# Kernel tuning notes

Measured on AMD Instinct MI355X. Metric: run time of the kernel, lower is better.

Reference implementation:

```python
import jax, jax.numpy as jnp
import numpy as np

# ---- static configuration (matches init_kwargs) ----
B = 32
H = 56
W = 56
C = 192
HEADS = 6
WS = 7            # window size
SHIFT = 3         # shift size (WS // 2)
MLP_HIDDEN = 768  # 4 * C
CPB = 256         # clip(56*56//16, 256, 1024)
N = WS * WS       # tokens per window
NW = (H // WS) * (W // WS)  # windows per image
EPS = 1e-5

# ---- static tables (Swin V2 continuous relative position bias) ----
# log-spaced relative coords table: [(2*WS-1)^2, 2]
_r = np.arange(-(WS - 1), WS, dtype=np.float32)
_tab = np.stack(np.meshgrid(_r, _r, indexing='ij'), axis=-1)  # [2WS-1, 2WS-1, 2]
_tab = _tab / (WS - 1) * 8.0  # pretrained_window_size=0 -> use window_size-1
_tab = np.sign(_tab) * np.log2(np.abs(_tab) + 1.0) / np.log2(8.0)
REL_TABLE = jnp.asarray(_tab.reshape(-1, 2))

# relative position index: [N, N] into the (2WS-1)^2 table
_coords = np.stack(np.meshgrid(np.arange(WS), np.arange(WS), indexing='ij'))
_cf = _coords.reshape(2, -1)
_rel = (_cf[:, :, None] - _cf[:, None, :]).transpose(1, 2, 0).astype(np.int64)
_rel[..., 0] += WS - 1
_rel[..., 1] += WS - 1
_rel[..., 0] *= 2 * WS - 1
REL_INDEX = jnp.asarray(_rel.sum(-1))

# shifted-window attention mask: [NW, N, N] with 0 / -100
_img = np.zeros((H, W), dtype=np.float32)
_sl = [slice(0, -WS), slice(-WS, -SHIFT), slice(-SHIFT, None)]
_cnt = 0
for _hs in _sl:
    for _ws in _sl:
        _img[_hs, _ws] = _cnt
        _cnt += 1
_mw = _img.reshape(H // WS, WS, W // WS, WS).transpose(0, 2, 1, 3).reshape(-1, N)
_am = _mw[:, None, :] - _mw[:, :, None]
ATTN_MASK = jnp.asarray(np.where(_am != 0, -100.0, 0.0).astype(np.float32))


def _layer_norm(x, g, b):
    mu = jnp.mean(x, axis=-1, keepdims=True)
    var = jnp.mean(jnp.square(x - mu), axis=-1, keepdims=True)
    return (x - mu) * jax.lax.rsqrt(var + EPS) * g + b


def setup_inputs() -> dict:
    key = jax.random.key(0)
    ks = jax.random.split(key, 10)
    def n(k, shape, s=0.02):
        return jax.random.normal(k, shape, jnp.float32) * s
    return {
        'x': jax.random.normal(ks[0], (B, H * W, C), jnp.float32),
        'qkv_w': n(ks[1], (3 * C, C)),
        'q_bias': jnp.zeros((C,), jnp.float32),
        'v_bias': jnp.zeros((C,), jnp.float32),
        'logit_scale': jnp.full((HEADS, 1, 1), jnp.log(10.0), jnp.float32),
        'cpb_w1': n(ks[2], (CPB, 2)),
        'cpb_b1': jnp.zeros((CPB,), jnp.float32),
        'cpb_w2': n(ks[3], (HEADS, CPB)),
        'proj_w': n(ks[4], (C, C)),
        'proj_b': jnp.zeros((C,), jnp.float32),
        'norm1_g': jnp.ones((C,), jnp.float32),
        'norm1_b': jnp.zeros((C,), jnp.float32),
        'norm2_g': jnp.ones((C,), jnp.float32),
        'norm2_b': jnp.zeros((C,), jnp.float32),
        'fc1_w': n(ks[5], (MLP_HIDDEN, C)),
        'fc1_b': jnp.zeros((MLP_HIDDEN,), jnp.float32),
        'fc2_w': n(ks[6], (C, MLP_HIDDEN)),
        'fc2_b': jnp.zeros((C,), jnp.float32),
    }


def reference(x, qkv_w, q_bias, v_bias, logit_scale, cpb_w1, cpb_b1, cpb_w2,
              proj_w, proj_b, norm1_g, norm1_b, norm2_g, norm2_b,
              fc1_w, fc1_b, fc2_w, fc2_b):
    b = x.shape[0]
    hd = C // HEADS
    shortcut = x

    # cyclic shift + window partition -> [b*NW, N, C]
    xi = jnp.roll(x.reshape(b, H, W, C), (-SHIFT, -SHIFT), axis=(1, 2))
    xw = xi.reshape(b, H // WS, WS, W // WS, WS, C)
    xw = xw.transpose(0, 1, 3, 2, 4, 5).reshape(-1, N, C)

    # qkv projection (k has no bias, per Swin V2)
    qkv_bias = jnp.concatenate([q_bias, jnp.zeros_like(q_bias), v_bias])
    qkv = (xw @ qkv_w.T + qkv_bias).reshape(-1, N, 3, HEADS, hd)
    qkv = qkv.transpose(2, 0, 3, 1, 4)  # [3, bw, heads, N, hd]
    q, k, v = qkv[0], qkv[1], qkv[2]

    # cosine attention with learned logit scale
    q = q / jnp.maximum(jnp.linalg.norm(q, axis=-1, keepdims=True), 1e-12)
    k = k / jnp.maximum(jnp.linalg.norm(k, axis=-1, keepdims=True), 1e-12)
    scale = jnp.exp(jnp.minimum(logit_scale, jnp.log(100.0)))  # [heads,1,1]
    attn = jnp.einsum('bhnd,bhmd->bhnm', q, k) * scale

    # continuous relative position bias via tiny MLP
    tab = jax.nn.relu(REL_TABLE @ cpb_w1.T + cpb_b1) @ cpb_w2.T  # [(2WS-1)^2, heads]
    rpb = 16.0 * jax.nn.sigmoid(tab[REL_INDEX])                  # [N, N, heads]
    attn = attn + rpb.transpose(2, 0, 1)[None]

    # shifted-window mask + softmax
    attn = attn.reshape(-1, NW, HEADS, N, N) + ATTN_MASK[None, :, None]
    attn = jax.nn.softmax(attn.reshape(-1, HEADS, N, N), axis=-1)

    out = jnp.einsum('bhnm,bhmd->bhnd', attn, v)
    out = out.transpose(0, 2, 1, 3).reshape(-1, N, C) @ proj_w.T + proj_b

    # window reverse + reverse shift
    xr = out.reshape(b, H // WS, W // WS, WS, WS, C)
    xr = xr.transpose(0, 1, 3, 2, 4, 5).reshape(b, H, W, C)
    xr = jnp.roll(xr, (SHIFT, SHIFT), axis=(1, 2)).reshape(b, H * W, C)

    # post-norm residual (Swin V2 style)
    x1 = shortcut + _layer_norm(xr, norm1_g, norm1_b)
    hmid = jax.nn.silu(x1 @ fc1_w.T + fc1_b) @ fc2_w.T + fc2_b
    return x1 + _layer_norm(hmid, norm2_g, norm2_b)
```

## Files before the change

### kernel.cpp

```cpp
#include <hip/hip_runtime.h>


typedef unsigned short ushort_t;
using f32x4  = __attribute__((ext_vector_type(4))) float;
using short8 = __attribute__((ext_vector_type(8))) short;

__device__ __forceinline__ ushort_t f2bf(float f) {
  union { float f; unsigned u; } v; v.f = f;
  unsigned r = v.u + 0x7fffu + ((v.u >> 16) & 1u);
  return (ushort_t)(r >> 16);
}
__device__ __forceinline__ float bf2f(ushort_t u) {
  union { unsigned u; float f; } v; v.u = ((unsigned)u) << 16;
  return v.f;
}

__device__ __forceinline__ int img_pos(int m) {
  int win = m / 49, n = m - win * 49;
  int b = win >> 6, wi = win & 63;
  int nd = n / 7, nm = n - nd * 7;
  int hs = (wi >> 3) * 7 + nd;
  int ws = (wi & 7) * 7 + nm;
  int h = hs + 3; if (h >= 56) h -= 56;
  int w = ws + 3; if (w >= 56) w -= 56;
  return b * 3136 + h * 56 + w;
}

__device__ __forceinline__ int region3(int a) { return a < 49 ? 0 : (a < 53 ? 1 : 2); }

__global__ void cvt_kernel(const float* __restrict__ in, ushort_t* __restrict__ out, int n) {
  int i = blockIdx.x * 256 + threadIdx.x;
  if (i < n) out[i] = f2bf(in[i]);
}

__global__ __launch_bounds__(256) void gather_cvt_kernel(
    const float* __restrict__ x, ushort_t* __restrict__ xw) {
  int i8 = blockIdx.x * 256 + threadIdx.x;
  int m = i8 / 24, c8 = (i8 - m * 24) * 8;
  const float* p = x + (size_t)img_pos(m) * 192 + c8;
  float4 a = *(const float4*)p, b = *(const float4*)(p + 4);
  ushort_t* q = xw + (size_t)m * 192 + c8;
  *(ushort4*)q       = make_ushort4(f2bf(a.x), f2bf(a.y), f2bf(a.z), f2bf(a.w));
  *(ushort4*)(q + 4) = make_ushort4(f2bf(b.x), f2bf(b.y), f2bf(b.z), f2bf(b.w));
}

__global__ __launch_bounds__(256) void cpb_kernel(
    const float* __restrict__ w1, const float* __restrict__ b1,
    const float* __restrict__ w2, float* __restrict__ tab_s) {
  int e = blockIdx.x;
  int t = threadIdx.x;
  int i = e / 13, j = e - 13 * (e / 13);
  auto cval = [](int a) -> float {
    float r = (a - 6) * (8.0f / 6.0f);
    float v = log2f(fabsf(r) + 1.f) * (1.f / 3.f);
    return r < 0.f ? -v : v;
  };
  float ci = cval(i), cj = cval(j);
  float h = fmaxf(ci * w1[2 * t] + cj * w1[2 * t + 1] + b1[t], 0.f);
  __shared__ float red[256];
  for (int head = 0; head < 6; ++head) {
    red[t] = h * w2[head * 256 + t];
    __syncthreads();
    for (int st = 128; st > 0; st >>= 1) {
      if (t < st) red[t] += red[t + st];
      __syncthreads();
    }
    if (t == 0) tab_s[head * 169 + e] = 16.f / (1.f + __expf(-red[0]));
    __syncthreads();
  }
}

template<int KTOT, int MODE>
__global__ __launch_bounds__(256) void gemm_n192(
    const ushort_t* __restrict__ Ab, const ushort_t* __restrict__ W,
    const float* __restrict__ b0, const float* __restrict__ b1,
    ushort_t* out, float* outf, int NTOT) {
  __shared__ ushort_t Al[128][40];
  __shared__ ushort_t Bl[192][40];
  int t = threadIdx.x;
  int m0 = blockIdx.x * 128, n0 = blockIdx.y * 192;

  int arow = t >> 1, akoff = (t & 1) << 4;
  const ushort_t* Arowp = Ab + (size_t)(m0 + arow) * KTOT + akoff;
  int colA = akoff ? 4 : 0;

  int lane = t & 63, wid = t >> 6;
  int wm = wid >> 1, wn = wid & 1;
  int lr = lane & 15, lg = lane >> 4;

  int bn = t >> 2, cB = t & 3;
  const ushort_t* Browp = W + (size_t)(n0 + bn) * KTOT + (cB << 3);
  const ushort_t* Browp2 = W + (size_t)(n0 + 64 + bn) * KTOT + (cB << 3);
  const ushort_t* Browp3 = W + (size_t)(n0 + 128 + bn) * KTOT + (cB << 3);
  int colB = ((cB & 1) << 4) | ((cB >> 1) << 2);

  f32x4 acc[4][6];
#pragma unroll
  for (int a = 0; a < 4; ++a)
#pragma unroll
    for (int b = 0; b < 6; ++b) acc[a][b] = (f32x4){0.f, 0.f, 0.f, 0.f};

  ushort4 a0, a1, a2, a3, bq0[2], bq1[2], bq2[2];
  auto LOADREGS = [&](int kt) {
    a0 = *(const ushort4*)(Arowp + kt + 0);
    a1 = *(const ushort4*)(Arowp + kt + 4);
    a2 = *(const ushort4*)(Arowp + kt + 8);
    a3 = *(const ushort4*)(Arowp + kt + 12);
    bq0[0] = *(const ushort4*)(Browp + kt);
    bq0[1] = *(const ushort4*)(Browp + kt + 4);
    bq1[0] = *(const ushort4*)(Browp2 + kt);
    bq1[1] = *(const ushort4*)(Browp2 + kt + 4);
    bq2[0] = *(const ushort4*)(Browp3 + kt);
    bq2[1] = *(const ushort4*)(Browp3 + kt + 4);
  };

  const int NT = KTOT / 32;
  LOADREGS(0);
  for (int it = 0; it < NT; ++it) {
    ushort_t* Ar = &Al[arow][0];
    *(ushort4*)(Ar + colA +  0) = a0;
    *(ushort4*)(Ar + colA +  8) = a1;
    *(ushort4*)(Ar + colA + 16) = a2;
    *(ushort4*)(Ar + colA + 24) = a3;
    ushort_t* Br0 = &Bl[bn][0];
    *(ushort4*)(Br0 + colB + 0) = bq0[0];
    *(ushort4*)(Br0 + colB + 8) = bq0[1];
    ushort_t* Br1 = &Bl[64 + bn][0];
    *(ushort4*)(Br1 + colB + 0) = bq1[0];
    *(ushort4*)(Br1 + colB + 8) = bq1[1];
    ushort_t* Br2 = &Bl[128 + bn][0];
    *(ushort4*)(Br2 + colB + 0) = bq2[0];
    *(ushort4*)(Br2 + colB + 8) = bq2[1];
    __syncthreads();
    if (it + 1 < NT) LOADREGS((it + 1) * 32);
    short8 af[4], bfv[6];
#pragma unroll
    for (int fm = 0; fm < 4; ++fm)
      af[fm] = *(const short8*)&Al[wm * 64 + fm * 16 + lr][lg * 8];
#pragma unroll
    for (int fn = 0; fn < 6; ++fn)
      bfv[fn] = *(const short8*)&Bl[wn * 96 + fn * 16 + lr][lg * 8];
#pragma unroll
    for (int fm = 0; fm < 4; ++fm)
#pragma unroll
      for (int fn = 0; fn < 6; ++fn)
        acc[fm][fn] = __builtin_amdgcn_mfma_f32_16x16x32_bf16(af[fm], bfv[fn], acc[fm][fn], 0, 0, 0);
    if (it + 1 < NT) __syncthreads();
  }
#pragma unroll
  for (int fm = 0; fm < 4; ++fm) {
#pragma unroll
    for (int fn = 0; fn < 6; ++fn) {
      int col = n0 + wn * 96 + fn * 16 + lr;
      float bias;
      if (MODE == 0) bias = (col < 192) ? b0[col] : ((col < 384) ? 0.f : b1[col - 384]);
      else           bias = b0[col];
#pragma unroll
      for (int r = 0; r < 4; ++r) {
        int row = m0 + wm * 64 + fm * 16 + lg * 4 + r;
        float v = acc[fm][fn][r] + bias;
        if (MODE == 1) v = v / (1.f + __expf(-v));
        if (MODE == 3) outf[(size_t)row * NTOT + col] = v;
        else           out[(size_t)row * NTOT + col] = f2bf(v);
      }
    }
  }
}

template<int MODE>
__global__ __launch_bounds__(256) void ln_resid_kernel(
    const ushort_t* __restrict__ pre, const float* __restrict__ residf,
    const ushort_t* __restrict__ residb, const float* __restrict__ gamma,
    const float* __restrict__ beta, ushort_t* __restrict__ outb,
    float* outio) {
  int m = (blockIdx.x * 256 + threadIdx.x) >> 6;
  int lane = threadIdx.x & 63;
  float v0, v1, v2;
  if (MODE == 0) {
    const ushort_t* p = pre + (size_t)m * 192;
    v0 = bf2f(p[lane]); v1 = bf2f(p[lane + 64]); v2 = bf2f(p[lane + 128]);
  } else {
    const float* p = outio + (size_t)m * 192;
    v0 = p[lane]; v1 = p[lane + 64]; v2 = p[lane + 128];
  }
  float s1 = v0 + v1 + v2;
  float s2 = v0 * v0 + v1 * v1 + v2 * v2;
#pragma unroll
  for (int o = 1; o < 64; o <<= 1) {
    s1 += __shfl_xor(s1, o);
    s2 += __shfl_xor(s2, o);
  }
  float mean = s1 * (1.f / 192.f);
  float var  = s2 * (1.f / 192.f) - mean * mean;
  float rstd = rsqrtf(fmaxf(var, 0.f) + 1e-5f);
  float l0 = (v0 - mean) * rstd * gamma[lane]       + beta[lane];
  float l1 = (v1 - mean) * rstd * gamma[lane + 64]  + beta[lane + 64];
  float l2 = (v2 - mean) * rstd * gamma[lane + 128] + beta[lane + 128];
  if (MODE == 0) {
    size_t og = (size_t)img_pos(m) * 192;
    outb[og + lane]       = f2bf(residf[og + lane]       + l0);
    outb[og + lane + 64]  = f2bf(residf[og + lane + 64]  + l1);
    outb[og + lane + 128] = f2bf(residf[og + lane + 128] + l2);
  } else {
    size_t og = (size_t)m * 192;
    outio[og + lane]       = bf2f(residb[og + lane])       + l0;
    outio[og + lane + 64]  = bf2f(residb[og + lane + 64])  + l1;
    outio[og + lane + 128] = bf2f(residb[og + lane + 128]) + l2;
  }
}

__global__ __launch_bounds__(256) void attn_kernel(
    const ushort_t* __restrict__ qkv, const float* __restrict__ logit_scale,
    const float* __restrict__ tab_s, ushort_t* __restrict__ attn_out) {
  __shared__ ushort_t qs[64][40];
  __shared__ ushort_t ksl[64][40];
  __shared__ ushort_t vsl[32][80];
  __shared__ ushort_t ps[64][80];
  __shared__ float tab_l[169];
  int win = blockIdx.x, head = blockIdx.y;
  int t = threadIdx.x;
  int wi = win & 63;
  int wh0 = (wi >> 3) * 7, ww0 = (wi & 7) * 7;
  size_t base = (size_t)win * 49 * 576 + head * 32;

  for (int u = t; u < 169; u += 256) tab_l[u] = tab_s[head * 169 + u];

  for (int u = t; u < 240; u += 256) {
    int arr = u / 120, v = u - arr * 120;
    int r = 49 + (v >> 3), c4 = (v & 7) << 2;
    ushort_t* p = arr ? &ksl[r][c4] : &qs[r][c4];
    *(ushort4*)p = make_ushort4(0, 0, 0, 0);
  }

  for (int u = t; u < 2048; u += 256) {
    int key = u >> 5, d = u & 31;
    ushort_t val = 0;
    if (key < 49) val = qkv[base + (size_t)key * 576 + 384 + d];
    int kk = key & 31;
    int pc = ((key >> 5) << 5) + 8 * ((kk >> 2) & 3) + 4 * (kk >> 4) + (kk & 3);
    vsl[d][pc] = val;
  }

  float scale = __expf(fminf(logit_scale[head], 4.605170186f));

  if (t < 196) {
    int r = t >> 2, c = t & 3;
    const ushort_t* qp = qkv + base + (size_t)r * 576 + c * 8;
    ushort4 qa = *(const ushort4*)qp,         qb = *(const ushort4*)(qp + 4);
    ushort4 ka = *(const ushort4*)(qp + 192), kb = *(const ushort4*)(qp + 196);
    float qf[8] = {bf2f(qa.x), bf2f(qa.y), bf2f(qa.z), bf2f(qa.w),
                   bf2f(qb.x), bf2f(qb.y), bf2f(qb.z), bf2f(qb.w)};
    float kf[8] = {bf2f(ka.x), bf2f(ka.y), bf2f(ka.z), bf2f(ka.w),
                   bf2f(kb.x), bf2f(kb.y), bf2f(kb.z), bf2f(kb.w)};
    float sq = 0.f, sk = 0.f;
#pragma unroll
    for (int d = 0; d < 8; ++d) { sq += qf[d] * qf[d]; sk += kf[d] * kf[d]; }
    sq += __shfl_xor(sq, 1); sq += __shfl_xor(sq, 2);
    sk += __shfl_xor(sk, 1); sk += __shfl_xor(sk, 2);
    float rq = scale / fmaxf(sqrtf(sq), 1e-12f);
    float rk = 1.f   / fmaxf(sqrtf(sk), 1e-12f);
    int c0 = ((c & 1) << 4) | ((c >> 1) << 2);
    ushort_t* qd = &qs[r][c0];
    *(ushort4*)(qd + 0) = make_ushort4(f2bf(qf[0]*rq), f2bf(qf[1]*rq), f2bf(qf[2]*rq), f2bf(qf[3]*rq));
    *(ushort4*)(qd + 8) = make_ushort4(f2bf(qf[4]*rq), f2bf(qf[5]*rq), f2bf(qf[6]*rq), f2bf(qf[7]*rq));
    ushort_t* kd = &ksl[r][c0];
    *(ushort4*)(kd + 0) = make_ushort4(f2bf(kf[0]*rk), f2bf(kf[1]*rk), f2bf(kf[2]*rk), f2bf(kf[3]*rk));
    *(ushort4*)(kd + 8) = make_ushort4(f2bf(kf[4]*rk), f2bf(kf[5]*rk), f2bf(kf[6]*rk), f2bf(kf[7]*rk));
  }
  __syncthreads();

  int lane = t & 63, w = t >> 6;
  int lr = lane & 15, lg = lane >> 4;

  short8 aq = *(const short8*)&qs[w * 16 + lr][lg * 8];
  f32x4 acc[4];
#pragma unroll
  for (int fn = 0; fn < 4; ++fn) {
    acc[fn] = (f32x4){0.f, 0.f, 0.f, 0.f};
    short8 bk = *(const short8*)&ksl[fn * 16 + lr][lg * 8];
    acc[fn] = __builtin_amdgcn_mfma_f32_16x16x32_bf16(aq, bk, acc[fn], 0, 0, 0);
  }

  float rsum[4];
#pragma unroll
  for (int r = 0; r < 4; ++r) {
    int row = w * 16 + lg * 4 + r;
    int rd = (row * 9363) >> 16, rm = row - 7 * rd;
    int gr = region3(wh0 + rd) * 3 + region3(ww0 + rm);
    bool rv = row < 49;
    float sv[4];
#pragma unroll
    for (int fn = 0; fn < 4; ++fn) {
      int col = fn * 16 + lr;
      int jd = (col * 9363) >> 16, jm = col - 7 * jd;
      int gj = region3(wh0 + jd) * 3 + region3(ww0 + jm);
      bool cv = rv && (col < 49);
      int idx = cv ? (rd - jd + 6) * 13 + (rm - jm + 6) : 0;
      float s = acc[fn][r] + tab_l[idx] + (gr == gj ? 0.f : -100.f);
      sv[fn] = cv ? s : -1e30f;
    }
    float m = fmaxf(fmaxf(sv[0], sv[1]), fmaxf(sv[2], sv[3]));
#pragma unroll
    for (int o = 1; o < 16; o <<= 1) m = fmaxf(m, __shfl_xor(m, o));
    float sum = 0.f;
#pragma unroll
    for (int fn = 0; fn < 4; ++fn) {
      float e = __expf(sv[fn] - m);
      sum += e;
      int pc = ((fn >> 1) << 5) + 8 * (lr >> 2) + ((fn & 1) << 2) + (lr & 3);
      ps[row][pc] = f2bf(e);
    }
#pragma unroll
    for (int o = 1; o < 16; o <<= 1) sum += __shfl_xor(sum, o);
    rsum[r] = 1.f / sum;
  }
  __syncthreads();

  short8 ap0 = *(const short8*)&ps[w * 16 + lr][lg * 8];
  short8 ap1 = *(const short8*)&ps[w * 16 + lr][32 + lg * 8];
  f32x4 o2[2];
#pragma unroll
  for (int f = 0; f < 2; ++f) {
    o2[f] = (f32x4){0.f, 0.f, 0.f, 0.f};
    short8 bv0 = *(const short8*)&vsl[f * 16 + lr][lg * 8];
    short8 bv1 = *(const short8*)&vsl[f * 16 + lr][32 + lg * 8];
    o2[f] = __builtin_amdgcn_mfma_f32_16x16x32_bf16(ap0, bv0, o2[f], 0, 0, 0);
    o2[f] = __builtin_amdgcn_mfma_f32_16x16x32_bf16(ap1, bv1, o2[f], 0, 0, 0);
  }
#pragma unroll
  for (int f = 0; f < 2; ++f) {
#pragma unroll
    for (int r = 0; r < 4; ++r) {
      int row = w * 16 + lg * 4 + r;
      if (row < 49)
        attn_out[((size_t)win * 49 + row) * 192 + head * 32 + f * 16 + lr] =
            f2bf(o2[f][r] * rsum[r]);
    }
  }
}

extern "C" void kernel_launch(void* const* d_in, const int* in_sizes, int n_in,
                              void* d_out, int out_size, void* d_ws, size_t ws_size,
                              hipStream_t stream) {
  (void)in_sizes; (void)n_in; (void)out_size; (void)ws_size;
  const float* x    = (const float*)d_in[0];
  const float* qkvw = (const float*)d_in[1];
  const float* qb   = (const float*)d_in[2];
  const float* vb   = (const float*)d_in[3];
  const float* ls   = (const float*)d_in[4];
  const float* cw1  = (const float*)d_in[5];
  const float* cb1  = (const float*)d_in[6];
  const float* cw2  = (const float*)d_in[7];
  const float* pw   = (const float*)d_in[8];
  const float* pb   = (const float*)d_in[9];
  const float* n1g  = (const float*)d_in[10];
  const float* n1b  = (const float*)d_in[11];
  const float* n2g  = (const float*)d_in[12];
  const float* n2b  = (const float*)d_in[13];
  const float* f1w  = (const float*)d_in[14];
  const float* f1b  = (const float*)d_in[15];
  const float* f2w  = (const float*)d_in[16];
  const float* f2b  = (const float*)d_in[17];
  float* out = (float*)d_out;

  char* ws = (char*)d_ws;
  ushort_t* wq_bf = (ushort_t*)ws;
  ushort_t* wp_bf = wq_bf + 110592;
  ushort_t* w1_bf = wp_bf + 36864;
  ushort_t* w2_bf = w1_bf + 147456;
  float*    tab_s = (float*)(w2_bf + 147456);
  const size_t OFF_BIG = 1 << 20;
  ushort_t* qkv_out = (ushort_t*)(ws + OFF_BIG);
  ushort_t* xw_bf   = (ushort_t*)(ws + OFF_BIG + 115605504);
  ushort_t* attn_o  = (ushort_t*)(ws + OFF_BIG + 115605504);
  ushort_t* x1_bf   = (ushort_t*)(ws + OFF_BIG + 154140672);
  ushort_t* hmid    = (ushort_t*)(ws + OFF_BIG);

  cvt_kernel<<<(110592 + 255) / 256, 256, 0, stream>>>(qkvw, wq_bf, 110592);
  cvt_kernel<<<(36864  + 255) / 256, 256, 0, stream>>>(pw,   wp_bf, 36864);
  cvt_kernel<<<(147456 + 255) / 256, 256, 0, stream>>>(f1w,  w1_bf, 147456);
  cvt_kernel<<<(147456 + 255) / 256, 256, 0, stream>>>(f2w,  w2_bf, 147456);
  cpb_kernel<<<169, 256, 0, stream>>>(cw1, cb1, cw2, tab_s);
  gather_cvt_kernel<<<9408, 256, 0, stream>>>(x, xw_bf);

  gemm_n192<192, 0><<<dim3(784, 3), 256, 0, stream>>>(xw_bf, wq_bf, qb, vb, qkv_out, nullptr, 576);
  attn_kernel<<<dim3(2048, 6), 256, 0, stream>>>(qkv_out, ls, tab_s, attn_o);
  gemm_n192<192, 2><<<dim3(784, 1), 256, 0, stream>>>(attn_o, wp_bf, pb, nullptr, attn_o, nullptr, 192);
  ln_resid_kernel<0><<<25088, 256, 0, stream>>>(attn_o, x, nullptr, n1g, n1b, x1_bf, nullptr);
  gemm_n192<192, 1><<<dim3(784, 4), 256, 0, stream>>>(x1_bf, w1_bf, f1b, nullptr, hmid, nullptr, 768);
  gemm_n192<768, 3><<<dim3(784, 1), 256, 0, stream>>>(hmid, w2_bf, f2b, nullptr, nullptr, out, 192);
  ln_resid_kernel<1><<<25088, 256, 0, stream>>>(nullptr, nullptr, x1_bf, n2g, n2b, nullptr, out);
}
```

Baseline: 422.3 us.

## Fuse MLP fc1+SiLU+fc2 into one kernel keeping hidden activations in LDS

Replaces the two MLP GEMM launches with a single fused kernel that computes fc1+SiLU in 192-column chunks into shared memory and immediately accumulates fc2 from it, so the 768-wide hidden tensor never goes to global memory. The fc2 weight is converted with a permuted K layout so the B fragments can be read directly from global memory in MFMA order. It removes a large hidden-activation write and read but uses 64-row tiles with 66 KB of LDS, which lowers occupancy, and it reads fc2 weights from global memory without staging them in shared memory.

```diff
diff --git a/kernel.cpp b/kernel.cpp
--- a/kernel.cpp
+++ b/kernel.cpp
@@ -31,6 +31,16 @@
 __global__ void cvt_kernel(const float* __restrict__ in, ushort_t* __restrict__ out, int n) {
   int i = blockIdx.x * 256 + threadIdx.x;
   if (i < n) out[i] = f2bf(in[i]);
+}
+
+__global__ void cvt_perm_kernel(const float* __restrict__ in, ushort_t* __restrict__ out,
+                                int n, int K) {
+  int i = blockIdx.x * 256 + threadIdx.x;
+  if (i >= n) return;
+  int row = i / K, j = i - row * K;
+  int k = j & 31;
+  int s = (j & ~31) + (((k & 15) >> 2) << 3) + ((k >> 4) << 2) + (k & 3);
+  out[row * K + s] = f2bf(in[i]);
 }
 
 __global__ __launch_bounds__(256) void gather_cvt_kernel(
@@ -162,6 +172,144 @@
         if (MODE == 1) v = v / (1.f + __expf(-v));
         if (MODE == 3) outf[(size_t)row * NTOT + col] = v;
         else           out[(size_t)row * NTOT + col] = f2bf(v);
+      }
+    }
+  }
+}
+
+#define APAD 200
+__global__ __launch_bounds__(256, 2) void mlp_fused_kernel(
+    const ushort_t* __restrict__ x1b, const ushort_t* __restrict__ w1p,
+    const ushort_t* __restrict__ w2p, const float* __restrict__ b1f,
+    const float* __restrict__ b2f, float* __restrict__ outf) {
+  extern __shared__ ushort_t smem[];
+  ushort_t* A_x1 = smem;
+  ushort_t* hidc = smem + 12800;
+  ushort_t* Bl   = smem + 25600;
+  int t = threadIdx.x;
+  int m0 = blockIdx.x * 64;
+  int lane = t & 63, wid = t >> 6;
+  int wm = wid >> 1, wn = wid & 1;
+  int lr = lane & 15, lg = lane >> 4;
+
+  for (int s = 0; s < 6; ++s) {
+    int task = t + (s << 8);
+    int row = task / 24, j = task - row * 24;
+    int c8 = j * 8;
+    const ushort_t* p = x1b + (size_t)(m0 + row) * 192 + c8;
+    ushort4 v0 = *(const ushort4*)p, v1 = *(const ushort4*)(p + 4);
+    int blk = c8 & ~31, jj = (c8 & 31) >> 3;
+    int b4 = ((jj & 1) << 4) | ((jj >> 1) << 2);
+    *(ushort4*)&A_x1[row * APAD + blk + b4]     = v0;
+    *(ushort4*)&A_x1[row * APAD + blk + b4 + 8] = v1;
+  }
+
+  int bn = t >> 2, cB = t & 3;
+  int colB = ((cB & 1) << 4) | ((cB >> 1) << 2);
+
+  f32x4 acc2[2][6];
+#pragma unroll
+  for (int a = 0; a < 2; ++a)
+#pragma unroll
+    for (int b = 0; b < 6; ++b) acc2[a][b] = (f32x4){0.f, 0.f, 0.f, 0.f};
+
+  __syncthreads();
+
+  for (int c = 0; c < 4; ++c) {
+    const ushort_t* Wc = w1p + (size_t)(c * 192) * 192;
+    const ushort_t* Br0p = Wc + (size_t)bn * 192 + (cB << 3);
+    const ushort_t* Br1p = Wc + (size_t)(64 + bn) * 192 + (cB << 3);
+    const ushort_t* Br2p = Wc + (size_t)(128 + bn) * 192 + (cB << 3);
+    ushort4 bq0[2], bq1[2], bq2[2];
+    auto LOADB = [&](int kt) {
+      bq0[0] = *(const ushort4*)(Br0p + kt); bq0[1] = *(const ushort4*)(Br0p + kt + 4);
+      bq1[0] = *(const ushort4*)(Br1p + kt); bq1[1] = *(const ushort4*)(Br1p + kt + 4);
+      bq2[0] = *(const ushort4*)(Br2p + kt); bq2[1] = *(const ushort4*)(Br2p + kt + 4);
+    };
+    f32x4 acc1[2][6];
+#pragma unroll
+    for (int a = 0; a < 2; ++a)
+#pragma unroll
+      for (int b = 0; b < 6; ++b) acc1[a][b] = (f32x4){0.f, 0.f, 0.f, 0.f};
+
+    LOADB(0);
+    for (int it = 0; it < 6; ++it) {
+      ushort_t* Br0 = &Bl[bn * 40];
+      *(ushort4*)(Br0 + colB + 0) = bq0[0];
+      *(ushort4*)(Br0 + colB + 8) = bq0[1];
+      ushort_t* Br1 = &Bl[(64 + bn) * 40];
+      *(ushort4*)(Br1 + colB + 0) = bq1[0];
+      *(ushort4*)(Br1 + colB + 8) = bq1[1];
+      ushort_t* Br2 = &Bl[(128 + bn) * 40];
+      *(ushort4*)(Br2 + colB + 0) = bq2[0];
+      *(ushort4*)(Br2 + colB + 8) = bq2[1];
+      __syncthreads();
+      if (it + 1 < 6) LOADB((it + 1) * 32);
+      short8 af[2], bfv[6];
+#pragma unroll
+      for (int fm = 0; fm < 2; ++fm)
+        af[fm] = *(const short8*)&A_x1[(wm * 32 + fm * 16 + lr) * APAD + it * 32 + lg * 8];
+#pragma unroll
+      for (int fn = 0; fn < 6; ++fn)
+        bfv[fn] = *(const short8*)&Bl[(wn * 96 + fn * 16 + lr) * 40 + lg * 8];
+#pragma unroll
+      for (int fm = 0; fm < 2; ++fm)
+#pragma unroll
+        for (int fn = 0; fn < 6; ++fn)
+          acc1[fm][fn] = __builtin_amdgcn_mfma_f32_16x16x32_bf16(af[fm], bfv[fn], acc1[fm][fn], 0, 0, 0);
+      __syncthreads();
+    }
+
+#pragma unroll
+    for (int fm = 0; fm < 2; ++fm) {
+#pragma unroll
+      for (int fn = 0; fn < 6; ++fn) {
+        int col = wn * 96 + fn * 16 + lr;
+        float bias = b1f[c * 192 + col];
+        int blk = (col >> 5) << 5, k5 = col & 31;
+        int slot = 8 * ((k5 & 15) >> 2) + ((k5 >> 4) << 2) + (k5 & 3);
+#pragma unroll
+        for (int r = 0; r < 4; ++r) {
+          int row = wm * 32 + fm * 16 + lg * 4 + r;
+          float v = acc1[fm][fn][r] + bias;
+          v = v / (1.f + __expf(-v));
+          hidc[row * APAD + blk + slot] = f2bf(v);
+        }
+      }
+    }
+    __syncthreads();
+
+    const ushort_t* W2c = w2p + (size_t)(c * 192);
+#pragma unroll
+    for (int i = 0; i < 6; ++i) {
+      short8 af2[2], bf2[6];
+#pragma unroll
+      for (int fm = 0; fm < 2; ++fm)
+        af2[fm] = *(const short8*)&hidc[(wm * 32 + fm * 16 + lr) * APAD + i * 32 + lg * 8];
+#pragma unroll
+      for (int fn = 0; fn < 6; ++fn) {
+        int col = wn * 96 + fn * 16 + lr;
+        bf2[fn] = *(const short8*)(W2c + (size_t)col * 768 + i * 32 + lg * 8);
+      }
+#pragma unroll
+      for (int fm = 0; fm < 2; ++fm)
+#pragma unroll
+        for (int fn = 0; fn < 6; ++fn)
+          acc2[fm][fn] = __builtin_amdgcn_mfma_f32_16x16x32_bf16(af2[fm], bf2[fn], acc2[fm][fn], 0, 0, 0);
+    }
+    __syncthreads();
+  }
+
+#pragma unroll
+  for (int fm = 0; fm < 2; ++fm) {
+#pragma unroll
+    for (int fn = 0; fn < 6; ++fn) {
+      int col = wn * 96 + fn * 16 + lr;
+      float bias = b2f[col];
+#pragma unroll
+      for (int r = 0; r < 4; ++r) {
+        int row = m0 + wm * 32 + fm * 16 + lg * 4 + r;
+        outf[(size_t)row * 192 + col] = acc2[fm][fn][r] + bias;
       }
     }
   }
@@ -374,12 +522,11 @@
   ushort_t* xw_bf   = (ushort_t*)(ws + OFF_BIG + 115605504);
   ushort_t* attn_o  = (ushort_t*)(ws + OFF_BIG + 115605504);
   ushort_t* x1_bf   = (ushort_t*)(ws + OFF_BIG + 154140672);
-  ushort_t* hmid    = (ushort_t*)(ws + OFF_BIG);
 
   cvt_kernel<<<(110592 + 255) / 256, 256, 0, stream>>>(qkvw, wq_bf, 110592);
   cvt_kernel<<<(36864  + 255) / 256, 256, 0, stream>>>(pw,   wp_bf, 36864);
   cvt_kernel<<<(147456 + 255) / 256, 256, 0, stream>>>(f1w,  w1_bf, 147456);
-  cvt_kernel<<<(147456 + 255) / 256, 256, 0, stream>>>(f2w,  w2_bf, 147456);
+  cvt_perm_kernel<<<(147456 + 255) / 256, 256, 0, stream>>>(f2w, w2_bf, 147456, 768);
   cpb_kernel<<<169, 256, 0, stream>>>(cw1, cb1, cw2, tab_s);
   gather_cvt_kernel<<<9408, 256, 0, stream>>>(x, xw_bf);
 
@@ -387,7 +534,6 @@
   attn_kernel<<<dim3(2048, 6), 256, 0, stream>>>(qkv_out, ls, tab_s, attn_o);
   gemm_n192<192, 2><<<dim3(784, 1), 256, 0, stream>>>(attn_o, wp_bf, pb, nullptr, attn_o, nullptr, 192);
   ln_resid_kernel<0><<<25088, 256, 0, stream>>>(attn_o, x, nullptr, n1g, n1b, x1_bf, nullptr);
-  gemm_n192<192, 1><<<dim3(784, 4), 256, 0, stream>>>(x1_bf, w1_bf, f1b, nullptr, hmid, nullptr, 768);
-  gemm_n192<768, 3><<<dim3(784, 1), 256, 0, stream>>>(hmid, w2_bf, f2b, nullptr, nullptr, out, 192);
+  mlp_fused_kernel<<<1568, 256, 66560, stream>>>(x1_bf, w1_bf, w2_bf, f1b, f2b, out);
   ln_resid_kernel<1><<<25088, 256, 0, stream>>>(nullptr, nullptr, x1_bf, n2g, n2b, nullptr, out);
 }
```

After: 485.9 us. 15.1% more time.

## Pre-permute QKV GEMM operands in global memory and load MFMA fragments directly

Applied to the files above, without the earlier changes.

The gather kernel and the QKV weight conversion now write bf16 data in a k-permuted order that matches the MFMA fragment layout. A new QKV GEMM kernel then loads A and B fragments straight from global memory with 16-byte loads, skipping LDS staging and the block barriers. The other GEMMs switch their staging loads from 8-byte to 16-byte loads. Each wave now issues redundant global loads for shared rows and relies on cache hits instead of LDS reuse.

```diff
diff --git a/kernel.cpp b/kernel.cpp
--- a/kernel.cpp
+++ b/kernel.cpp
@@ -4,6 +4,7 @@
 typedef unsigned short ushort_t;
 using f32x4  = __attribute__((ext_vector_type(4))) float;
 using short8 = __attribute__((ext_vector_type(8))) short;
+union LD16 { short8 v; ushort4 h[2]; };
 
 __device__ __forceinline__ ushort_t f2bf(float f) {
   union { float f; unsigned u; } v; v.f = f;
@@ -33,15 +34,28 @@
   if (i < n) out[i] = f2bf(in[i]);
 }
 
+__global__ void cvt_perm_kernel(const float* __restrict__ in, ushort_t* __restrict__ out,
+                                int n, int K) {
+  int i = blockIdx.x * 256 + threadIdx.x;
+  if (i >= n) return;
+  int row = i / K, j = i - row * K;
+  int k = j & 31;
+  int s = (j & ~31) + (((k & 15) >> 2) << 3) + ((k >> 4) << 2) + (k & 3);
+  out[row * K + s] = f2bf(in[i]);
+}
+
 __global__ __launch_bounds__(256) void gather_cvt_kernel(
     const float* __restrict__ x, ushort_t* __restrict__ xw) {
   int i8 = blockIdx.x * 256 + threadIdx.x;
   int m = i8 / 24, c8 = (i8 - m * 24) * 8;
   const float* p = x + (size_t)img_pos(m) * 192 + c8;
   float4 a = *(const float4*)p, b = *(const float4*)(p + 4);
-  ushort_t* q = xw + (size_t)m * 192 + c8;
-  *(ushort4*)q       = make_ushort4(f2bf(a.x), f2bf(a.y), f2bf(a.z), f2bf(a.w));
-  *(ushort4*)(q + 4) = make_ushort4(f2bf(b.x), f2bf(b.y), f2bf(b.z), f2bf(b.w));
+  ushort_t* q = xw + (size_t)m * 192;
+  int blk = c8 & ~31;
+  int jj = (c8 & 31) >> 3;
+  int b4 = ((jj & 1) << 4) | ((jj >> 1) << 2);
+  *(ushort4*)(q + blk + b4)     = make_ushort4(f2bf(a.x), f2bf(a.y), f2bf(a.z), f2bf(a.w));
+  *(ushort4*)(q + blk + b4 + 8) = make_ushort4(f2bf(b.x), f2bf(b.y), f2bf(b.z), f2bf(b.w));
 }
 
 __global__ __launch_bounds__(256) void cpb_kernel(
@@ -70,11 +84,63 @@
   }
 }
 
+__global__ __launch_bounds__(256) void gemm_direct_qkv(
+    const ushort_t* __restrict__ Ap, const ushort_t* __restrict__ Wp,
+    const float* __restrict__ b0, const float* __restrict__ b1,
+    ushort_t* __restrict__ out, int NTOT) {
+  int t = threadIdx.x;
+  int m0 = blockIdx.x * 128, n0 = blockIdx.y * 192;
+  int lane = t & 63, wid = t >> 6;
+  int wm = wid >> 1, wn = wid & 1;
+  int lr = lane & 15, lg = lane >> 4;
+
+  const ushort_t* ar[4];
+  const ushort_t* br[6];
+#pragma unroll
+  for (int fm = 0; fm < 4; ++fm)
+    ar[fm] = Ap + (size_t)(m0 + wm * 64 + fm * 16 + lr) * 192 + lg * 8;
+#pragma unroll
+  for (int fn = 0; fn < 6; ++fn)
+    br[fn] = Wp + (size_t)(n0 + wn * 96 + fn * 16 + lr) * 192 + lg * 8;
+
+  f32x4 acc[4][6];
+#pragma unroll
+  for (int a = 0; a < 4; ++a)
+#pragma unroll
+    for (int b = 0; b < 6; ++b) acc[a][b] = (f32x4){0.f, 0.f, 0.f, 0.f};
+
+#pragma unroll
+  for (int kt = 0; kt < 192; kt += 32) {
+    short8 af[4], bfv[6];
+#pragma unroll
+    for (int fm = 0; fm < 4; ++fm) af[fm] = *(const short8*)(ar[fm] + kt);
+#pragma unroll
+    for (int fn = 0; fn < 6; ++fn) bfv[fn] = *(const short8*)(br[fn] + kt);
+#pragma unroll
+    for (int fm = 0; fm < 4; ++fm)
+#pragma unroll
+      for (int fn = 0; fn < 6; ++fn)
+        acc[fm][fn] = __builtin_amdgcn_mfma_f32_16x16x32_bf16(af[fm], bfv[fn], acc[fm][fn], 0, 0, 0);
+  }
+#pragma unroll
+  for (int fm = 0; fm < 4; ++fm) {
+#pragma unroll
+    for (int fn = 0; fn < 6; ++fn) {
+      int col = n0 + wn * 96 + fn * 16 + lr;
+      float bias = (col < 192) ? b0[col] : ((col < 384) ? 0.f : b1[col - 384]);
+#pragma unroll
+      for (int r = 0; r < 4; ++r) {
+        int row = m0 + wm * 64 + fm * 16 + lg * 4 + r;
+        out[(size_t)row * NTOT + col] = f2bf(acc[fm][fn][r] + bias);
+      }
+    }
+  }
+}
+
 template<int KTOT, int MODE>
 __global__ __launch_bounds__(256) void gemm_n192(
     const ushort_t* __restrict__ Ab, const ushort_t* __restrict__ W,
-    const float* __restrict__ b0, const float* __restrict__ b1,
-    ushort_t* out, float* outf, int NTOT) {
+    const float* __restrict__ b0, ushort_t* out, float* outf, int NTOT) {
   __shared__ ushort_t Al[128][40];
   __shared__ ushort_t Bl[192][40];
   int t = threadIdx.x;
@@ -89,7 +155,7 @@
   int lr = lane & 15, lg = lane >> 4;
 
   int bn = t >> 2, cB = t & 3;
-  const ushort_t* Browp = W + (size_t)(n0 + bn) * KTOT + (cB << 3);
+  const ushort_t* Browp  = W + (size_t)(n0 + bn) * KTOT + (cB << 3);
   const ushort_t* Browp2 = W + (size_t)(n0 + 64 + bn) * KTOT + (cB << 3);
   const ushort_t* Browp3 = W + (size_t)(n0 + 128 + bn) * KTOT + (cB << 3);
   int colB = ((cB & 1) << 4) | ((cB >> 1) << 2);
@@ -100,37 +166,32 @@
 #pragma unroll
     for (int b = 0; b < 6; ++b) acc[a][b] = (f32x4){0.f, 0.f, 0.f, 0.f};
 
-  ushort4 a0, a1, a2, a3, bq0[2], bq1[2], bq2[2];
+  LD16 A01, A23, B0, B1, B2;
   auto LOADREGS = [&](int kt) {
-    a0 = *(const ushort4*)(Arowp + kt + 0);
-    a1 = *(const ushort4*)(Arowp + kt + 4);
-    a2 = *(const ushort4*)(Arowp + kt + 8);
-    a3 = *(const ushort4*)(Arowp + kt + 12);
-    bq0[0] = *(const ushort4*)(Browp + kt);
-    bq0[1] = *(const ushort4*)(Browp + kt + 4);
-    bq1[0] = *(const ushort4*)(Browp2 + kt);
-    bq1[1] = *(const ushort4*)(Browp2 + kt + 4);
-    bq2[0] = *(const ushort4*)(Browp3 + kt);
-    bq2[1] = *(const ushort4*)(Browp3 + kt + 4);
+    A01.v = *(const short8*)(Arowp + kt);
+    A23.v = *(const short8*)(Arowp + kt + 8);
+    B0.v  = *(const short8*)(Browp + kt);
+    B1.v  = *(const short8*)(Browp2 + kt);
+    B2.v  = *(const short8*)(Browp3 + kt);
   };
 
   const int NT = KTOT / 32;
   LOADREGS(0);
   for (int it = 0; it < NT; ++it) {
     ushort_t* Ar = &Al[arow][0];
-    *(ushort4*)(Ar + colA +  0) = a0;
-    *(ushort4*)(Ar + colA +  8) = a1;
-    *(ushort4*)(Ar + colA + 16) = a2;
-    *(ushort4*)(Ar + colA + 24) = a3;
+    *(ushort4*)(Ar + colA +  0) = A01.h[0];
+    *(ushort4*)(Ar + colA +  8) = A01.h[1];
+    *(ushort4*)(Ar + colA + 16) = A23.h[0];
+    *(ushort4*)(Ar + colA + 24) = A23.h[1];
     ushort_t* Br0 = &Bl[bn][0];
-    *(ushort4*)(Br0 + colB + 0) = bq0[0];
-    *(ushort4*)(Br0 + colB + 8) = bq0[1];
+    *(ushort4*)(Br0 + colB + 0) = B0.h[0];
+    *(ushort4*)(Br0 + colB + 8) = B0.h[1];
     ushort_t* Br1 = &Bl[64 + bn][0];
-    *(ushort4*)(Br1 + colB + 0) = bq1[0];
-    *(ushort4*)(Br1 + colB + 8) = bq1[1];
+    *(ushort4*)(Br1 + colB + 0) = B1.h[0];
+    *(ushort4*)(Br1 + colB + 8) = B1.h[1];
     ushort_t* Br2 = &Bl[128 + bn][0];
-    *(ushort4*)(Br2 + colB + 0) = bq2[0];
-    *(ushort4*)(Br2 + colB + 8) = bq2[1];
+    *(ushort4*)(Br2 + colB + 0) = B2.h[0];
+    *(ushort4*)(Br2 + colB + 8) = B2.h[1];
     __syncthreads();
     if (it + 1 < NT) LOADREGS((it + 1) * 32);
     short8 af[4], bfv[6];
@@ -152,9 +213,7 @@
 #pragma unroll
     for (int fn = 0; fn < 6; ++fn) {
       int col = n0 + wn * 96 + fn * 16 + lr;
-      float bias;
-      if (MODE == 0) bias = (col < 192) ? b0[col] : ((col < 384) ? 0.f : b1[col - 384]);
-      else           bias = b0[col];
+      float bias = b0[col];
 #pragma unroll
       for (int r = 0; r < 4; ++r) {
         int row = m0 + wm * 64 + fm * 16 + lg * 4 + r;
@@ -376,18 +435,18 @@
   ushort_t* x1_bf   = (ushort_t*)(ws + OFF_BIG + 154140672);
   ushort_t* hmid    = (ushort_t*)(ws + OFF_BIG);
 
-  cvt_kernel<<<(110592 + 255) / 256, 256, 0, stream>>>(qkvw, wq_bf, 110592);
+  cvt_perm_kernel<<<(110592 + 255) / 256, 256, 0, stream>>>(qkvw, wq_bf, 110592, 192);
   cvt_kernel<<<(36864  + 255) / 256, 256, 0, stream>>>(pw,   wp_bf, 36864);
   cvt_kernel<<<(147456 + 255) / 256, 256, 0, stream>>>(f1w,  w1_bf, 147456);
   cvt_kernel<<<(147456 + 255) / 256, 256, 0, stream>>>(f2w,  w2_bf, 147456);
   cpb_kernel<<<169, 256, 0, stream>>>(cw1, cb1, cw2, tab_s);
   gather_cvt_kernel<<<9408, 256, 0, stream>>>(x, xw_bf);
 
-  gemm_n192<192, 0><<<dim3(784, 3), 256, 0, stream>>>(xw_bf, wq_bf, qb, vb, qkv_out, nullptr, 576);
+  gemm_direct_qkv<<<dim3(784, 3), 256, 0, stream>>>(xw_bf, wq_bf, qb, vb, qkv_out, 576);
   attn_kernel<<<dim3(2048, 6), 256, 0, stream>>>(qkv_out, ls, tab_s, attn_o);
-  gemm_n192<192, 2><<<dim3(784, 1), 256, 0, stream>>>(attn_o, wp_bf, pb, nullptr, attn_o, nullptr, 192);
+  gemm_n192<192, 2><<<dim3(784, 1), 256, 0, stream>>>(attn_o, wp_bf, pb, attn_o, nullptr, 192);
   ln_resid_kernel<0><<<25088, 256, 0, stream>>>(attn_o, x, nullptr, n1g, n1b, x1_bf, nullptr);
-  gemm_n192<192, 1><<<dim3(784, 4), 256, 0, stream>>>(x1_bf, w1_bf, f1b, nullptr, hmid, nullptr, 768);
-  gemm_n192<768, 3><<<dim3(784, 1), 256, 0, stream>>>(hmid, w2_bf, f2b, nullptr, nullptr, out, 192);
+  gemm_n192<192, 1><<<dim3(784, 4), 256, 0, stream>>>(x1_bf, w1_bf, f1b, hmid, nullptr, 768);
+  gemm_n192<768, 3><<<dim3(784, 1), 256, 0, stream>>>(hmid, w2_bf, f2b, nullptr, out, 192);
   ln_resid_kernel<1><<<25088, 256, 0, stream>>>(nullptr, nullptr, x1_bf, n2g, n2b, nullptr, out);
 }
```

Result: slower. 445.4 us (+5.5%).

## Use 512-thread GEMM blocks with 8 waves, half-tile accumulators, 16-byte loads

Applied to the files above, without the earlier changes.

The GEMM block grows from 4 to 8 waves. Each wave now computes a 32x96 sub-tile instead of 64x96, which halves the accumulator registers and aims for more waves per CU to hide latency. Only the first 256 threads stage global tiles into LDS, now with 16-byte loads in place of pairs of 8-byte loads. The trade-off is that half the threads sit idle during staging, and each block does more barrier synchronisation relative to its MFMA work.

```diff
diff --git a/kernel.cpp b/kernel.cpp
--- a/kernel.cpp
+++ b/kernel.cpp
@@ -4,6 +4,7 @@
 typedef unsigned short ushort_t;
 using f32x4  = __attribute__((ext_vector_type(4))) float;
 using short8 = __attribute__((ext_vector_type(8))) short;
+union LD16 { short8 v; ushort4 h[2]; };
 
 __device__ __forceinline__ ushort_t f2bf(float f) {
   union { float f; unsigned u; } v; v.f = f;
@@ -71,7 +72,7 @@
 }
 
 template<int KTOT, int MODE>
-__global__ __launch_bounds__(256) void gemm_n192(
+__global__ __launch_bounds__(512, 4) void gemm_n192(
     const ushort_t* __restrict__ Ab, const ushort_t* __restrict__ W,
     const float* __restrict__ b0, const float* __restrict__ b1,
     ushort_t* out, float* outf, int NTOT) {
@@ -79,76 +80,72 @@
   __shared__ ushort_t Bl[192][40];
   int t = threadIdx.x;
   int m0 = blockIdx.x * 128, n0 = blockIdx.y * 192;
-
-  int arow = t >> 1, akoff = (t & 1) << 4;
-  const ushort_t* Arowp = Ab + (size_t)(m0 + arow) * KTOT + akoff;
-  int colA = akoff ? 4 : 0;
-
   int lane = t & 63, wid = t >> 6;
   int wm = wid >> 1, wn = wid & 1;
   int lr = lane & 15, lg = lane >> 4;
 
-  int bn = t >> 2, cB = t & 3;
-  const ushort_t* Browp = W + (size_t)(n0 + bn) * KTOT + (cB << 3);
+  bool stager = (t < 256);
+  int arow = (t & 255) >> 1, akoff = (t & 1) << 4;
+  const ushort_t* Arowp = Ab + (size_t)(m0 + arow) * KTOT + akoff;
+  int colA = akoff ? 4 : 0;
+  int bn = (t & 255) >> 2, cB = t & 3;
+  const ushort_t* Browp  = W + (size_t)(n0 + bn) * KTOT + (cB << 3);
   const ushort_t* Browp2 = W + (size_t)(n0 + 64 + bn) * KTOT + (cB << 3);
   const ushort_t* Browp3 = W + (size_t)(n0 + 128 + bn) * KTOT + (cB << 3);
   int colB = ((cB & 1) << 4) | ((cB >> 1) << 2);
 
-  f32x4 acc[4][6];
-#pragma unroll
-  for (int a = 0; a < 4; ++a)
+  f32x4 acc[2][6];
+#pragma unroll
+  for (int a = 0; a < 2; ++a)
 #pragma unroll
     for (int b = 0; b < 6; ++b) acc[a][b] = (f32x4){0.f, 0.f, 0.f, 0.f};
 
-  ushort4 a0, a1, a2, a3, bq0[2], bq1[2], bq2[2];
+  LD16 A01, A23, B0, B1, B2;
   auto LOADREGS = [&](int kt) {
-    a0 = *(const ushort4*)(Arowp + kt + 0);
-    a1 = *(const ushort4*)(Arowp + kt + 4);
-    a2 = *(const ushort4*)(Arowp + kt + 8);
-    a3 = *(const ushort4*)(Arowp + kt + 12);
-    bq0[0] = *(const ushort4*)(Browp + kt);
-    bq0[1] = *(const ushort4*)(Browp + kt + 4);
-    bq1[0] = *(const ushort4*)(Browp2 + kt);
-    bq1[1] = *(const ushort4*)(Browp2 + kt + 4);
-    bq2[0] = *(const ushort4*)(Browp3 + kt);
-    bq2[1] = *(const ushort4*)(Browp3 + kt + 4);
+    A01.v = *(const short8*)(Arowp + kt);
+    A23.v = *(const short8*)(Arowp + kt + 8);
+    B0.v  = *(const short8*)(Browp + kt);
+    B1.v  = *(const short8*)(Browp2 + kt);
+    B2.v  = *(const short8*)(Browp3 + kt);
   };
 
   const int NT = KTOT / 32;
-  LOADREGS(0);
+  if (stager) LOADREGS(0);
   for (int it = 0; it < NT; ++it) {
-    ushort_t* Ar = &Al[arow][0];
-    *(ushort4*)(Ar + colA +  0) = a0;
-    *(ushort4*)(Ar + colA +  8) = a1;
-    *(ushort4*)(Ar + colA + 16) = a2;
-    *(ushort4*)(Ar + colA + 24) = a3;
-    ushort_t* Br0 = &Bl[bn][0];
-    *(ushort4*)(Br0 + colB + 0) = bq0[0];
-    *(ushort4*)(Br0 + colB + 8) = bq0[1];
-    ushort_t* Br1 = &Bl[64 + bn][0];
-    *(ushort4*)(Br1 + colB + 0) = bq1[0];
-    *(ushort4*)(Br1 + colB + 8) = bq1[1];
-    ushort_t* Br2 = &Bl[128 + bn][0];
-    *(ushort4*)(Br2 + colB + 0) = bq2[0];
-    *(ushort4*)(Br2 + colB + 8) = bq2[1];
+    if (stager) {
+      ushort_t* Ar = &Al[arow][0];
+      *(ushort4*)(Ar + colA +  0) = A01.h[0];
+      *(ushort4*)(Ar + colA +  8) = A01.h[1];
+      *(ushort4*)(Ar + colA + 16) = A23.h[0];
+      *(ushort4*)(Ar + colA + 24) = A23.h[1];
+      ushort_t* Br0 = &Bl[bn][0];
+      *(ushort4*)(Br0 + colB + 0) = B0.h[0];
+      *(ushort4*)(Br0 + colB + 8) = B0.h[1];
+      ushort_t* Br1 = &Bl[64 + bn][0];
+      *(ushort4*)(Br1 + colB + 0) = B1.h[0];
+      *(ushort4*)(Br1 + colB + 8) = B1.h[1];
+      ushort_t* Br2 = &Bl[128 + bn][0];
+      *(ushort4*)(Br2 + colB + 0) = B2.h[0];
+      *(ushort4*)(Br2 + colB + 8) = B2.h[1];
+    }
     __syncthreads();
-    if (it + 1 < NT) LOADREGS((it + 1) * 32);
-    short8 af[4], bfv[6];
-#pragma unroll
-    for (int fm = 0; fm < 4; ++fm)
-      af[fm] = *(const short8*)&Al[wm * 64 + fm * 16 + lr][lg * 8];
+    if (stager && it + 1 < NT) LOADREGS((it + 1) * 32);
+    short8 af[2], bfv[6];
+#pragma unroll
+    for (int fm = 0; fm < 2; ++fm)
+      af[fm] = *(const short8*)&Al[wm * 32 + fm * 16 + lr][lg * 8];
 #pragma unroll
     for (int fn = 0; fn < 6; ++fn)
       bfv[fn] = *(const short8*)&Bl[wn * 96 + fn * 16 + lr][lg * 8];
 #pragma unroll
-    for (int fm = 0; fm < 4; ++fm)
+    for (int fm = 0; fm < 2; ++fm)
 #pragma unroll
       for (int fn = 0; fn < 6; ++fn)
         acc[fm][fn] = __builtin_amdgcn_mfma_f32_16x16x32_bf16(af[fm], bfv[fn], acc[fm][fn], 0, 0, 0);
     if (it + 1 < NT) __syncthreads();
   }
 #pragma unroll
-  for (int fm = 0; fm < 4; ++fm) {
+  for (int fm = 0; fm < 2; ++fm) {
 #pragma unroll
     for (int fn = 0; fn < 6; ++fn) {
       int col = n0 + wn * 96 + fn * 16 + lr;
@@ -157,7 +154,7 @@
       else           bias = b0[col];
 #pragma unroll
       for (int r = 0; r < 4; ++r) {
-        int row = m0 + wm * 64 + fm * 16 + lg * 4 + r;
+        int row = m0 + wm * 32 + fm * 16 + lg * 4 + r;
         float v = acc[fm][fn][r] + bias;
         if (MODE == 1) v = v / (1.f + __expf(-v));
         if (MODE == 3) outf[(size_t)row * NTOT + col] = v;
@@ -383,11 +380,11 @@
   cpb_kernel<<<169, 256, 0, stream>>>(cw1, cb1, cw2, tab_s);
   gather_cvt_kernel<<<9408, 256, 0, stream>>>(x, xw_bf);
 
-  gemm_n192<192, 0><<<dim3(784, 3), 256, 0, stream>>>(xw_bf, wq_bf, qb, vb, qkv_out, nullptr, 576);
+  gemm_n192<192, 0><<<dim3(784, 3), 512, 0, stream>>>(xw_bf, wq_bf, qb, vb, qkv_out, nullptr, 576);
   attn_kernel<<<dim3(2048, 6), 256, 0, stream>>>(qkv_out, ls, tab_s, attn_o);
-  gemm_n192<192, 2><<<dim3(784, 1), 256, 0, stream>>>(attn_o, wp_bf, pb, nullptr, attn_o, nullptr, 192);
+  gemm_n192<192, 2><<<dim3(784, 1), 512, 0, stream>>>(attn_o, wp_bf, pb, nullptr, attn_o, nullptr, 192);
   ln_resid_kernel<0><<<25088, 256, 0, stream>>>(attn_o, x, nullptr, n1g, n1b, x1_bf, nullptr);
-  gemm_n192<192, 1><<<dim3(784, 4), 256, 0, stream>>>(x1_bf, w1_bf, f1b, nullptr, hmid, nullptr, 768);
-  gemm_n192<768, 3><<<dim3(784, 1), 256, 0, stream>>>(hmid, w2_bf, f2b, nullptr, nullptr, out, 192);
+  gemm_n192<192, 1><<<dim3(784, 4), 512, 0, stream>>>(x1_bf, w1_bf, f1b, nullptr, hmid, nullptr, 768);
+  gemm_n192<768, 3><<<dim3(784, 1), 512, 0, stream>>>(hmid, w2_bf, f2b, nullptr, nullptr, out, 192);
   ln_resid_kernel<1><<<25088, 256, 0, stream>>>(nullptr, nullptr, x1_bf, n2g, n2b, nullptr, out);
 }
```

Result: faster. 402.7 us (-4.6%).
